# Optimization experiments

Measured on AMD Instinct MI355X. Metric: run time of the kernel, lower is better.

## Reference

```python
import jax, jax.numpy as jnp
import numpy as np

MARGIN = 0.3
N, D = 8192, 256
NUM_IDS = 1000


def setup_inputs() -> dict:
    key = jax.random.key(0)
    k1, k2 = jax.random.split(key)
    inputs = jax.random.normal(k1, (N, D), dtype=jnp.float32)
    targets = jax.random.randint(k2, (N,), 0, NUM_IDS, dtype=jnp.int64)
    return {"inputs": inputs, "targets": targets}


def reference(inputs, targets):
    # sim_mat[i, j] = <x_i, x_j>
    sim = jnp.matmul(inputs, inputs.T)  # [n, n]
    same = targets[:, None] == targets[None, :]  # [n, n] bool
    # positives: same label AND sim < 1 (note: strict; diagonal included only if ||x||^2 < 1)
    pos_mask = same & (sim < 1.0)
    # negatives: different label AND sim > margin
    neg_mask = (~same) & (sim > MARGIN)
    pos_loss = jnp.sum(jnp.where(pos_mask, 1.0 - sim, 0.0), axis=1)  # [n]
    neg_loss = jnp.sum(jnp.where(neg_mask, sim, 0.0), axis=1)  # [n]
    n = inputs.shape[0]
    return jnp.sum(pos_loss + neg_loss) / n
```

## Files before the change

kernel.cpp:

```cpp
#include <hip/hip_runtime.h>
#include <hip/hip_bf16.h>


#define MARGINF 0.3f

typedef __attribute__((ext_vector_type(8))) short short8x;
typedef __attribute__((ext_vector_type(16))) float f32x16;

__device__ __forceinline__ unsigned short f2bf(float f) {
    unsigned int u = __float_as_uint(f);
    unsigned int r = (u + 0x7fffu + ((u >> 16) & 1u)) >> 16;
    return (unsigned short)r;
}

__global__ void __launch_bounds__(256) convert_k(const float* __restrict__ x,
                                                 unsigned short* __restrict__ xb) {
    int i = blockIdx.x * 256 + threadIdx.x;
    const float4* p = reinterpret_cast<const float4*>(x) + (size_t)i * 2;
    float4 a = p[0];
    float4 b = p[1];
    short8x o;
    o[0] = (short)f2bf(a.x); o[1] = (short)f2bf(a.y);
    o[2] = (short)f2bf(a.z); o[3] = (short)f2bf(a.w);
    o[4] = (short)f2bf(b.x); o[5] = (short)f2bf(b.y);
    o[6] = (short)f2bf(b.z); o[7] = (short)f2bf(b.w);
    reinterpret_cast<short8x*>(xb)[i] = o;
}

__global__ void __launch_bounds__(256, 3) gemm_loss_k(const unsigned short* __restrict__ xb,
                                                      double* __restrict__ partials) {
    const int p = blockIdx.x;
    int bi = (int)(64.5f - sqrtf(64.5f * 64.5f - 2.0f * (float)p));
    if (bi < 0) bi = 0;
    if (bi > 63) bi = 63;
    while (bi > 0 && (bi * (129 - bi)) / 2 > p) --bi;
    while (((bi + 1) * (128 - bi)) / 2 <= p) ++bi;
    const int bj = bi + (p - (bi * (129 - bi)) / 2);

    __shared__ __align__(16) char ldsb[3 * 16384];
    __shared__ float redbuf[4];

    const int tid  = threadIdx.x;
    const int lane = tid & 63;
    const int wid  = tid >> 6;
    const int wr   = wid >> 1;
    const int wc   = wid & 1;

    const char* aBase = (const char*)(xb + (size_t)bi * 128 * 256);
    const char* bBase = (const char*)(xb + (size_t)bj * 128 * 256);

    const int srow0  = wid * 16 + (lane >> 2);
    const int schunk = (((lane & 3) ^ ((lane >> 3) & 3))) << 4;

    const int l31 = lane & 31;
    const int hi  = lane >> 5;
    const int swz = (l31 >> 1) & 3;
    int offA[2][2], offB[2][2];
#pragma unroll
    for (int fm = 0; fm < 2; ++fm)
#pragma unroll
        for (int ks = 0; ks < 2; ++ks)
            offA[fm][ks] = (wr * 64 + fm * 32 + l31) * 64 + ((((ks << 1) | hi) ^ swz) << 4);
#pragma unroll
    for (int fn = 0; fn < 2; ++fn)
#pragma unroll
        for (int ks = 0; ks < 2; ++ks)
            offB[fn][ks] = 8192 + (wc * 64 + fn * 32 + l31) * 64 + ((((ks << 1) | hi) ^ swz) << 4);

    f32x16 acc00 = {}, acc01 = {}, acc10 = {}, acc11 = {};

#define STAGE_KT(BUF, T) do {                                                        \
    _Pragma("unroll")                                                                \
    for (int i_ = 0; i_ < 2; ++i_) {                                                 \
        const int r_ = i_ * 64 + srow0;                                              \
        const char* sa_ = aBase + (size_t)r_ * 512 + (T) * 64 + schunk;              \
        const char* sb_ = bBase + (size_t)r_ * 512 + (T) * 64 + schunk;              \
        __builtin_amdgcn_global_load_lds(                                            \
            (const __attribute__((address_space(1))) unsigned int*)sa_,              \
            (__attribute__((address_space(3))) unsigned int*)(ldsb + (BUF) * 16384 + i_ * 4096 + wid * 1024), \
            16, 0, 0);                                                               \
        __builtin_amdgcn_global_load_lds(                                            \
            (const __attribute__((address_space(1))) unsigned int*)sb_,              \
            (__attribute__((address_space(3))) unsigned int*)(ldsb + (BUF) * 16384 + 8192 + i_ * 4096 + wid * 1024), \
            16, 0, 0);                                                               \
    }                                                                                \
} while (0)

#define GEMM_ITER(T, BUF, VMSTR, DOSTAGE) do {                                       \
    asm volatile("s_waitcnt vmcnt(" VMSTR ")" ::: "memory");                         \
    __builtin_amdgcn_s_barrier();                     \
    const char* lb_ = ldsb + (BUF) * 16384;                                          \
    short8x a0k0 = *(const short8x*)(lb_ + offA[0][0]);                              \
    short8x a1k0 = *(const short8x*)(lb_ + offA[1][0]);                              \
    short8x b0k0 = *(const short8x*)(lb_ + offB[0][0]);                              \
    short8x b1k0 = *(const short8x*)(lb_ + offB[1][0]);                              \
    short8x a0k1 = *(const short8x*)(lb_ + offA[0][1]);                              \
    short8x a1k1 = *(const short8x*)(lb_ + offA[1][1]);                              \
    short8x b0k1 = *(const short8x*)(lb_ + offB[0][1]);                              \
    short8x b1k1 = *(const short8x*)(lb_ + offB[1][1]);                              \
    asm volatile("s_waitcnt lgkmcnt(0)" ::: "memory");                               \
    __builtin_amdgcn_sched_barrier(0);                                               \
    __builtin_amdgcn_s_barrier();                    \
    if (DOSTAGE) STAGE_KT(BUF, (T) + 3);                    \
    __builtin_amdgcn_s_setprio(1);                                                   \
    acc00 = __builtin_amdgcn_mfma_f32_32x32x16_bf16(a0k0, b0k0, acc00, 0, 0, 0);     \
    acc01 = __builtin_amdgcn_mfma_f32_32x32x16_bf16(a0k0, b1k0, acc01, 0, 0, 0);     \
    acc10 = __builtin_amdgcn_mfma_f32_32x32x16_bf16(a1k0, b0k0, acc10, 0, 0, 0);     \
    acc11 = __builtin_amdgcn_mfma_f32_32x32x16_bf16(a1k0, b1k0, acc11, 0, 0, 0);     \
    acc00 = __builtin_amdgcn_mfma_f32_32x32x16_bf16(a0k1, b0k1, acc00, 0, 0, 0);     \
    acc01 = __builtin_amdgcn_mfma_f32_32x32x16_bf16(a0k1, b1k1, acc01, 0, 0, 0);     \
    acc10 = __builtin_amdgcn_mfma_f32_32x32x16_bf16(a1k1, b0k1, acc10, 0, 0, 0);     \
    acc11 = __builtin_amdgcn_mfma_f32_32x32x16_bf16(a1k1, b1k1, acc11, 0, 0, 0);     \
    __builtin_amdgcn_s_setprio(0);                                                   \
} while (0)

    STAGE_KT(0, 0);
    STAGE_KT(1, 1);
    STAGE_KT(2, 2);

    GEMM_ITER(0, 0, "8", 1);
    GEMM_ITER(1, 1, "8", 1);
    GEMM_ITER(2, 2, "8", 1);
    GEMM_ITER(3, 0, "8", 1);
    GEMM_ITER(4, 1, "8", 1);
    GEMM_ITER(5, 2, "8", 0);
    GEMM_ITER(6, 0, "4", 0);
    GEMM_ITER(7, 1, "0", 0);

#undef GEMM_ITER
#undef STAGE_KT

    float lsum = 0.f;
#pragma unroll
    for (int r = 0; r < 16; ++r) {
        float s;
        s = acc00[r]; lsum += (s > MARGINF) ? s : 0.0f;
        s = acc01[r]; lsum += (s > MARGINF) ? s : 0.0f;
        s = acc10[r]; lsum += (s > MARGINF) ? s : 0.0f;
        s = acc11[r]; lsum += (s > MARGINF) ? s : 0.0f;
    }
    if (bi != bj) lsum *= 2.0f;

#pragma unroll
    for (int mask = 1; mask < 64; mask <<= 1) lsum += __shfl_xor(lsum, mask, 64);
    if (lane == 0) redbuf[wid] = lsum;
    __syncthreads();
    if (tid == 0)
        partials[p] = (double)(redbuf[0] + redbuf[1] + redbuf[2] + redbuf[3]);
}

__global__ void __launch_bounds__(256) samepair_k(const unsigned short* __restrict__ xb,
                                                  const int* __restrict__ tg,
                                                  double* __restrict__ partials2) {
    const int lbl = blockIdx.x;
    __shared__ int idx[96];
    __shared__ int cnt;
    __shared__ double dred[4];
    if (threadIdx.x == 0) cnt = 0;
    __syncthreads();
    for (int i = threadIdx.x; i < 8192; i += 256)
        if (tg[i] == lbl) { int q = atomicAdd(&cnt, 1); if (q < 96) idx[q] = i; }
    __syncthreads();
    int c = cnt; if (c > 96) c = 96;

    double dsum = 0.0;
    for (int t = threadIdx.x; t < c * c; t += 256) {
        const int i = idx[t / c], j = idx[t % c];
        const short8x* xi = (const short8x*)(xb + (size_t)i * 256);
        const short8x* xj = (const short8x*)(xb + (size_t)j * 256);
        float s = 0.f;
#pragma unroll 4
        for (int q = 0; q < 32; ++q) {
            short8x a = xi[q], b = xj[q];
#pragma unroll
            for (int e = 0; e < 8; ++e) {
                float fa = __uint_as_float(((unsigned int)(unsigned short)a[e]) << 16);
                float fb = __uint_as_float(((unsigned int)(unsigned short)b[e]) << 16);
                s = fmaf(fa, fb, s);
            }
        }
        const float posv = (s < 1.0f) ? (1.0f - s) : 0.0f;
        const float negv = (s > MARGINF) ? s : 0.0f;
        dsum += (double)(posv - negv);
    }

#pragma unroll
    for (int mask = 1; mask < 64; mask <<= 1) dsum += __shfl_xor(dsum, mask, 64);
    const int wid = threadIdx.x >> 6;
    if ((threadIdx.x & 63) == 0) dred[wid] = dsum;
    __syncthreads();
    if (threadIdx.x == 0)
        partials2[lbl] = dred[0] + dred[1] + dred[2] + dred[3];
}

__global__ void __launch_bounds__(256) finalize_k(const double* __restrict__ partials,
                                                  float* __restrict__ out) {
    double s = 0.0;
    for (int i = threadIdx.x; i < 3080; i += 256) s += partials[i];
#pragma unroll
    for (int mask = 1; mask < 64; mask <<= 1) s += __shfl_xor(s, mask, 64);
    __shared__ double red[4];
    const int wid = threadIdx.x >> 6;
    if ((threadIdx.x & 63) == 0) red[wid] = s;
    __syncthreads();
    if (threadIdx.x == 0)
        out[0] = (float)((red[0] + red[1] + red[2] + red[3]) / 8192.0);
}

extern "C" void kernel_launch(void* const* d_in, const int* in_sizes, int n_in,
                              void* d_out, int out_size, void* d_ws, size_t ws_size,
                              hipStream_t stream) {
    (void)in_sizes; (void)n_in; (void)out_size; (void)ws_size;
    const float* x  = (const float*)d_in[0];
    const int*   tg = (const int*)d_in[1];
    float* out = (float*)d_out;

    double* partials   = (double*)d_ws;
    double* partials2  = (double*)d_ws + 2080;
    unsigned short* xb = (unsigned short*)((char*)d_ws + 32768);

    convert_k<<<1024, 256, 0, stream>>>(x, xb);
    gemm_loss_k<<<2080, 256, 0, stream>>>(xb, partials);
    samepair_k<<<1000, 256, 0, stream>>>(xb, tg, partials2);
    finalize_k<<<1, 256, 0, stream>>>(partials, out);
}
```

Baseline: 110.4 us.

## Use 256x256 triangular tiles with 512-thread blocks and wave-per-pair samepair dot

The GEMM tile grows from 128x128 to 256x256 over the upper triangle, giving 528 blocks of 8 waves with a 4x2 MFMA fragment grid per wave. It uses K-tiles of 64 with double-buffered 64KB LDS stages and an XCD-aware block remap. This is meant to raise operand reuse and cut global and LDS traffic per MFMA. In exchange, fewer blocks run at once and the tail may be less balanced. The same-label kernel now computes each dot product with one wave using a shuffle reduction, and its label-count cap rises to 128.

```diff
diff --git a/kernel.cpp b/kernel.cpp
--- a/kernel.cpp
+++ b/kernel.cpp
@@ -11,6 +11,9 @@
     unsigned int u = __float_as_uint(f);
     unsigned int r = (u + 0x7fffu + ((u >> 16) & 1u)) >> 16;
     return (unsigned short)r;
+}
+__device__ __forceinline__ float bf2f(unsigned short u) {
+    return __uint_as_float(((unsigned int)u) << 16);
 }
 
 __global__ void __launch_bounds__(256) convert_k(const float* __restrict__ x,
@@ -27,167 +30,170 @@
     reinterpret_cast<short8x*>(xb)[i] = o;
 }
 
-__global__ void __launch_bounds__(256, 3) gemm_loss_k(const unsigned short* __restrict__ xb,
+__global__ void __launch_bounds__(512, 2) gemm_loss_k(const unsigned short* __restrict__ xb,
                                                       double* __restrict__ partials) {
-    const int p = blockIdx.x;
-    int bi = (int)(64.5f - sqrtf(64.5f * 64.5f - 2.0f * (float)p));
+    const int praw = blockIdx.x;
+    const int p = (praw & 7) * 66 + (praw >> 3);
+    int bi = (int)(32.5f - sqrtf(32.5f * 32.5f - 2.0f * (float)p));
     if (bi < 0) bi = 0;
-    if (bi > 63) bi = 63;
-    while (bi > 0 && (bi * (129 - bi)) / 2 > p) --bi;
-    while (((bi + 1) * (128 - bi)) / 2 <= p) ++bi;
-    const int bj = bi + (p - (bi * (129 - bi)) / 2);
-
-    __shared__ __align__(16) char ldsb[3 * 16384];
-    __shared__ float redbuf[4];
+    if (bi > 31) bi = 31;
+    while (bi > 0 && (bi * (65 - bi)) / 2 > p) --bi;
+    while (((bi + 1) * (64 - bi)) / 2 <= p) ++bi;
+    const int bj = bi + (p - (bi * (65 - bi)) / 2);
+
+    __shared__ __align__(16) char ldsb[2 * 65536];
+    __shared__ float redbuf[8];
 
     const int tid  = threadIdx.x;
     const int lane = tid & 63;
     const int wid  = tid >> 6;
-    const int wr   = wid >> 1;
-    const int wc   = wid & 1;
-
-    const char* aBase = (const char*)(xb + (size_t)bi * 128 * 256);
-    const char* bBase = (const char*)(xb + (size_t)bj * 128 * 256);
-
-    const int srow0  = wid * 16 + (lane >> 2);
-    const int schunk = (((lane & 3) ^ ((lane >> 3) & 3))) << 4;
+    const int wr   = wid >> 2;
+    const int wc   = wid & 3;
+
+    const char* aBase = (const char*)(xb + (size_t)bi * 256 * 256);
+    const char* bBase = (const char*)(xb + (size_t)bj * 256 * 256);
+
+    const int srow   = tid >> 3;
+    const int schunk = ((tid & 7) ^ (srow & 7)) << 4;
 
     const int l31 = lane & 31;
     const int hi  = lane >> 5;
-    const int swz = (l31 >> 1) & 3;
-    int offA[2][2], offB[2][2];
-#pragma unroll
-    for (int fm = 0; fm < 2; ++fm)
-#pragma unroll
-        for (int ks = 0; ks < 2; ++ks)
-            offA[fm][ks] = (wr * 64 + fm * 32 + l31) * 64 + ((((ks << 1) | hi) ^ swz) << 4);
-#pragma unroll
-    for (int fn = 0; fn < 2; ++fn)
-#pragma unroll
-        for (int ks = 0; ks < 2; ++ks)
-            offB[fn][ks] = 8192 + (wc * 64 + fn * 32 + l31) * 64 + ((((ks << 1) | hi) ^ swz) << 4);
-
-    f32x16 acc00 = {}, acc01 = {}, acc10 = {}, acc11 = {};
-
-#define STAGE_KT(BUF, T) do {                                                        \
-    _Pragma("unroll")                                                                \
-    for (int i_ = 0; i_ < 2; ++i_) {                                                 \
-        const int r_ = i_ * 64 + srow0;                                              \
-        const char* sa_ = aBase + (size_t)r_ * 512 + (T) * 64 + schunk;              \
-        const char* sb_ = bBase + (size_t)r_ * 512 + (T) * 64 + schunk;              \
-        __builtin_amdgcn_global_load_lds(                                            \
-            (const __attribute__((address_space(1))) unsigned int*)sa_,              \
-            (__attribute__((address_space(3))) unsigned int*)(ldsb + (BUF) * 16384 + i_ * 4096 + wid * 1024), \
-            16, 0, 0);                                                               \
-        __builtin_amdgcn_global_load_lds(                                            \
-            (const __attribute__((address_space(1))) unsigned int*)sb_,              \
-            (__attribute__((address_space(3))) unsigned int*)(ldsb + (BUF) * 16384 + 8192 + i_ * 4096 + wid * 1024), \
-            16, 0, 0);                                                               \
-    }                                                                                \
+    const int s7  = l31 & 7;
+    int rA[4], rB[2], xc[4];
+#pragma unroll
+    for (int fm = 0; fm < 4; ++fm) rA[fm] = (wr * 128 + fm * 32 + l31) * 128;
+#pragma unroll
+    for (int fn = 0; fn < 2; ++fn) rB[fn] = 65536 / 2 + (wc * 64 + fn * 32 + l31) * 128;
+#pragma unroll
+    for (int ks = 0; ks < 4; ++ks) xc[ks] = (((2 * ks + hi) ^ s7) << 4);
+
+    f32x16 acc[4][2] = {};
+
+#define STAGE_KT(BUF, T) do {                                                         \
+    _Pragma("unroll")                                                                 \
+    for (int is_ = 0; is_ < 4; ++is_) {                                               \
+        const size_t gr_ = (size_t)(is_ * 64 + srow);                                 \
+        const char* sa_ = aBase + gr_ * 512 + (T) * 128 + schunk;                     \
+        const char* sb_ = bBase + gr_ * 512 + (T) * 128 + schunk;                     \
+        __builtin_amdgcn_global_load_lds(                                             \
+            (const __attribute__((address_space(1))) unsigned int*)sa_,               \
+            (__attribute__((address_space(3))) unsigned int*)(ldsb + (BUF) * 65536 + is_ * 8192 + tid * 16), \
+            16, 0, 0);                                                                \
+        __builtin_amdgcn_global_load_lds(                                             \
+            (const __attribute__((address_space(1))) unsigned int*)sb_,               \
+            (__attribute__((address_space(3))) unsigned int*)(ldsb + (BUF) * 65536 + 32768 + is_ * 8192 + tid * 16), \
+            16, 0, 0);                                                                \
+    }                                                                                 \
 } while (0)
 
-#define GEMM_ITER(T, BUF, VMSTR, DOSTAGE) do {                                       \
-    asm volatile("s_waitcnt vmcnt(" VMSTR ")" ::: "memory");                         \
+#define GEMM_ITER(T, BUF, VMSTR, DOSTAGE) do {                                        \
+    asm volatile("s_waitcnt vmcnt(" VMSTR ")" ::: "memory");                          \
+    __builtin_amdgcn_s_barrier();                           \
+    const char* lb_ = ldsb + (BUF) * 65536;                                           \
+    _Pragma("unroll")                                                                 \
+    for (int ks = 0; ks < 3; ++ks) {                                                  \
+        short8x af[4], bf[2];                                                         \
+        _Pragma("unroll")                                                             \
+        for (int fm = 0; fm < 4; ++fm) af[fm] = *(const short8x*)(lb_ + rA[fm] + xc[ks]); \
+        _Pragma("unroll")                                                             \
+        for (int fn = 0; fn < 2; ++fn) bf[fn] = *(const short8x*)(lb_ + rB[fn] + xc[ks]); \
+        _Pragma("unroll")                                                             \
+        for (int fm = 0; fm < 4; ++fm)                                                \
+            _Pragma("unroll")                                                         \
+            for (int fn = 0; fn < 2; ++fn)                                            \
+                acc[fm][fn] = __builtin_amdgcn_mfma_f32_32x32x16_bf16(af[fm], bf[fn], acc[fm][fn], 0, 0, 0); \
+    }                                                                                 \
+    short8x af3[4], bf3[2];                                                           \
+    _Pragma("unroll")                                                                 \
+    for (int fm = 0; fm < 4; ++fm) af3[fm] = *(const short8x*)(lb_ + rA[fm] + xc[3]); \
+    _Pragma("unroll")                                                                 \
+    for (int fn = 0; fn < 2; ++fn) bf3[fn] = *(const short8x*)(lb_ + rB[fn] + xc[3]); \
+    asm volatile("s_waitcnt lgkmcnt(0)" ::: "memory");                                \
+    __builtin_amdgcn_sched_barrier(0);                                                \
     __builtin_amdgcn_s_barrier();                     \
-    const char* lb_ = ldsb + (BUF) * 16384;                                          \
-    short8x a0k0 = *(const short8x*)(lb_ + offA[0][0]);                              \
-    short8x a1k0 = *(const short8x*)(lb_ + offA[1][0]);                              \
-    short8x b0k0 = *(const short8x*)(lb_ + offB[0][0]);                              \
-    short8x b1k0 = *(const short8x*)(lb_ + offB[1][0]);                              \
-    short8x a0k1 = *(const short8x*)(lb_ + offA[0][1]);                              \
-    short8x a1k1 = *(const short8x*)(lb_ + offA[1][1]);                              \
-    short8x b0k1 = *(const short8x*)(lb_ + offB[0][1]);                              \
-    short8x b1k1 = *(const short8x*)(lb_ + offB[1][1]);                              \
-    asm volatile("s_waitcnt lgkmcnt(0)" ::: "memory");                               \
-    __builtin_amdgcn_sched_barrier(0);                                               \
-    __builtin_amdgcn_s_barrier();                    \
-    if (DOSTAGE) STAGE_KT(BUF, (T) + 3);                    \
-    __builtin_amdgcn_s_setprio(1);                                                   \
-    acc00 = __builtin_amdgcn_mfma_f32_32x32x16_bf16(a0k0, b0k0, acc00, 0, 0, 0);     \
-    acc01 = __builtin_amdgcn_mfma_f32_32x32x16_bf16(a0k0, b1k0, acc01, 0, 0, 0);     \
-    acc10 = __builtin_amdgcn_mfma_f32_32x32x16_bf16(a1k0, b0k0, acc10, 0, 0, 0);     \
-    acc11 = __builtin_amdgcn_mfma_f32_32x32x16_bf16(a1k0, b1k0, acc11, 0, 0, 0);     \
-    acc00 = __builtin_amdgcn_mfma_f32_32x32x16_bf16(a0k1, b0k1, acc00, 0, 0, 0);     \
-    acc01 = __builtin_amdgcn_mfma_f32_32x32x16_bf16(a0k1, b1k1, acc01, 0, 0, 0);     \
-    acc10 = __builtin_amdgcn_mfma_f32_32x32x16_bf16(a1k1, b0k1, acc10, 0, 0, 0);     \
-    acc11 = __builtin_amdgcn_mfma_f32_32x32x16_bf16(a1k1, b1k1, acc11, 0, 0, 0);     \
-    __builtin_amdgcn_s_setprio(0);                                                   \
+    if (DOSTAGE) STAGE_KT(BUF, (T) + 2);                     \
+    __builtin_amdgcn_s_setprio(1);                                                    \
+    _Pragma("unroll")                                                                 \
+    for (int fm = 0; fm < 4; ++fm)                                                    \
+        _Pragma("unroll")                                                             \
+        for (int fn = 0; fn < 2; ++fn)                                                \
+            acc[fm][fn] = __builtin_amdgcn_mfma_f32_32x32x16_bf16(af3[fm], bf3[fn], acc[fm][fn], 0, 0, 0); \
+    __builtin_amdgcn_s_setprio(0);                                                    \
 } while (0)
 
     STAGE_KT(0, 0);
     STAGE_KT(1, 1);
-    STAGE_KT(2, 2);
 
     GEMM_ITER(0, 0, "8", 1);
     GEMM_ITER(1, 1, "8", 1);
-    GEMM_ITER(2, 2, "8", 1);
-    GEMM_ITER(3, 0, "8", 1);
-    GEMM_ITER(4, 1, "8", 1);
-    GEMM_ITER(5, 2, "8", 0);
-    GEMM_ITER(6, 0, "4", 0);
-    GEMM_ITER(7, 1, "0", 0);
+    GEMM_ITER(2, 0, "8", 0);
+    GEMM_ITER(3, 1, "0", 0);
 
 #undef GEMM_ITER
 #undef STAGE_KT
 
     float lsum = 0.f;
 #pragma unroll
-    for (int r = 0; r < 16; ++r) {
-        float s;
-        s = acc00[r]; lsum += (s > MARGINF) ? s : 0.0f;
-        s = acc01[r]; lsum += (s > MARGINF) ? s : 0.0f;
-        s = acc10[r]; lsum += (s > MARGINF) ? s : 0.0f;
-        s = acc11[r]; lsum += (s > MARGINF) ? s : 0.0f;
-    }
+    for (int fm = 0; fm < 4; ++fm)
+#pragma unroll
+        for (int fn = 0; fn < 2; ++fn)
+#pragma unroll
+            for (int r = 0; r < 16; ++r) {
+                const float s = acc[fm][fn][r];
+                lsum += (s > MARGINF) ? s : 0.0f;
+            }
     if (bi != bj) lsum *= 2.0f;
 
 #pragma unroll
     for (int mask = 1; mask < 64; mask <<= 1) lsum += __shfl_xor(lsum, mask, 64);
     if (lane == 0) redbuf[wid] = lsum;
     __syncthreads();
-    if (tid == 0)
-        partials[p] = (double)(redbuf[0] + redbuf[1] + redbuf[2] + redbuf[3]);
+    if (tid == 0) {
+        float t = 0.f;
+#pragma unroll
+        for (int w = 0; w < 8; ++w) t += redbuf[w];
+        partials[blockIdx.x] = (double)t;
+    }
 }
 
 __global__ void __launch_bounds__(256) samepair_k(const unsigned short* __restrict__ xb,
                                                   const int* __restrict__ tg,
                                                   double* __restrict__ partials2) {
     const int lbl = blockIdx.x;
-    __shared__ int idx[96];
+    __shared__ int idx[128];
     __shared__ int cnt;
     __shared__ double dred[4];
     if (threadIdx.x == 0) cnt = 0;
     __syncthreads();
     for (int i = threadIdx.x; i < 8192; i += 256)
-        if (tg[i] == lbl) { int q = atomicAdd(&cnt, 1); if (q < 96) idx[q] = i; }
-    __syncthreads();
-    int c = cnt; if (c > 96) c = 96;
-
+        if (tg[i] == lbl) { int q = atomicAdd(&cnt, 1); if (q < 128) idx[q] = i; }
+    __syncthreads();
+    int c = cnt; if (c > 128) c = 128;
+
+    const int wid  = threadIdx.x >> 6;
+    const int lane = threadIdx.x & 63;
     double dsum = 0.0;
-    for (int t = threadIdx.x; t < c * c; t += 256) {
+
+    for (int t = wid; t < c * c; t += 4) {
         const int i = idx[t / c], j = idx[t % c];
-        const short8x* xi = (const short8x*)(xb + (size_t)i * 256);
-        const short8x* xj = (const short8x*)(xb + (size_t)j * 256);
-        float s = 0.f;
-#pragma unroll 4
-        for (int q = 0; q < 32; ++q) {
-            short8x a = xi[q], b = xj[q];
-#pragma unroll
-            for (int e = 0; e < 8; ++e) {
-                float fa = __uint_as_float(((unsigned int)(unsigned short)a[e]) << 16);
-                float fb = __uint_as_float(((unsigned int)(unsigned short)b[e]) << 16);
-                s = fmaf(fa, fb, s);
-            }
+        const ushort4* ri = (const ushort4*)(xb + (size_t)i * 256);
+        const ushort4* rj = (const ushort4*)(xb + (size_t)j * 256);
+        ushort4 a = ri[lane];
+        ushort4 b = rj[lane];
+        float s = bf2f(a.x) * bf2f(b.x);
+        s = fmaf(bf2f(a.y), bf2f(b.y), s);
+        s = fmaf(bf2f(a.z), bf2f(b.z), s);
+        s = fmaf(bf2f(a.w), bf2f(b.w), s);
+#pragma unroll
+        for (int mask = 1; mask < 64; mask <<= 1) s += __shfl_xor(s, mask, 64);
+        if (lane == 0) {
+            const float posv = (s < 1.0f) ? (1.0f - s) : 0.0f;
+            const float negv = (s > MARGINF) ? s : 0.0f;
+            dsum += (double)(posv - negv);
         }
-        const float posv = (s < 1.0f) ? (1.0f - s) : 0.0f;
-        const float negv = (s > MARGINF) ? s : 0.0f;
-        dsum += (double)(posv - negv);
     }
 
-#pragma unroll
-    for (int mask = 1; mask < 64; mask <<= 1) dsum += __shfl_xor(dsum, mask, 64);
-    const int wid = threadIdx.x >> 6;
-    if ((threadIdx.x & 63) == 0) dred[wid] = dsum;
+    if (lane == 0) dred[wid] = dsum;
     __syncthreads();
     if (threadIdx.x == 0)
         partials2[lbl] = dred[0] + dred[1] + dred[2] + dred[3];
@@ -196,7 +202,7 @@
 __global__ void __launch_bounds__(256) finalize_k(const double* __restrict__ partials,
                                                   float* __restrict__ out) {
     double s = 0.0;
-    for (int i = threadIdx.x; i < 3080; i += 256) s += partials[i];
+    for (int i = threadIdx.x; i < 1528; i += 256) s += partials[i];
 #pragma unroll
     for (int mask = 1; mask < 64; mask <<= 1) s += __shfl_xor(s, mask, 64);
     __shared__ double red[4];
@@ -216,11 +222,11 @@
     float* out = (float*)d_out;
 
     double* partials   = (double*)d_ws;
-    double* partials2  = (double*)d_ws + 2080;
+    double* partials2  = (double*)d_ws + 528;
     unsigned short* xb = (unsigned short*)((char*)d_ws + 32768);
 
     convert_k<<<1024, 256, 0, stream>>>(x, xb);
-    gemm_loss_k<<<2080, 256, 0, stream>>>(xb, partials);
+    gemm_loss_k<<<528, 512, 0, stream>>>(xb, partials);
     samepair_k<<<1000, 256, 0, stream>>>(xb, tg, partials2);
     finalize_k<<<1, 256, 0, stream>>>(partials, out);
 }
```

After: 131.4 us. 1.19x slower.
